# Performance work log

Measured on AMD Instinct MI355X. Metric: run time of the kernel, lower is better.

The kernel has to match this reference:

```python
import jax, jax.numpy as jnp
import numpy as np

GROUP_SIZE = 128

def dequantize(imatrix, scales, zeros, group_size, out_dtype):
    # repeat group-wise scales/zeros along axis 0 to full weight shape
    rs = jnp.repeat(scales, group_size, axis=0)
    rz = jnp.repeat(zeros, group_size, axis=0)
    return ((imatrix.astype(rs.dtype) - rz.astype(rs.dtype)) * rs).astype(out_dtype)

def setup_inputs() -> dict:
    key = jax.random.key(0)
    ks = jax.random.split(key, 10)
    H, I, G = 4096, 14336, GROUP_SIZE
    B, S = 4, 2048
    x = jax.random.normal(ks[0], (B, S, H), dtype=jnp.float32)
    gate_w = jax.random.randint(ks[1], (H, I), 0, 16, dtype=jnp.int32)
    gate_z = jax.random.randint(ks[2], (H // G, I), 0, 16, dtype=jnp.int32)
    gate_s = jax.random.uniform(ks[3], (H // G, I), dtype=jnp.float32) * 0.01
    up_w = jax.random.randint(ks[4], (H, I), 0, 16, dtype=jnp.int32)
    up_z = jax.random.randint(ks[5], (H // G, I), 0, 16, dtype=jnp.int32)
    up_s = jax.random.uniform(ks[6], (H // G, I), dtype=jnp.float32) * 0.01
    down_w = jax.random.randint(ks[7], (I, H), 0, 16, dtype=jnp.int32)
    down_z = jax.random.randint(ks[8], (I // G, H), 0, 16, dtype=jnp.int32)
    down_s = jax.random.uniform(ks[9], (I // G, H), dtype=jnp.float32) * 0.01
    return {"x": x, "gate_w": gate_w, "gate_z": gate_z, "gate_s": gate_s,
            "up_w": up_w, "up_z": up_z, "up_s": up_s,
            "down_w": down_w, "down_z": down_z, "down_s": down_s}

def reference(x, gate_w, gate_z, gate_s, up_w, up_z, up_s, down_w, down_z, down_s):
    dt = x.dtype
    gate_proj = dequantize(gate_w, gate_s, gate_z, GROUP_SIZE, dt)  # [H, I]
    up_proj = dequantize(up_w, up_s, up_z, GROUP_SIZE, dt)          # [H, I]
    down_proj = dequantize(down_w, down_s, down_z, GROUP_SIZE, dt)  # [I, H]
    gate = jax.nn.silu(jnp.dot(x, gate_proj))  # [B, S, I]
    up = jnp.dot(x, up_proj)                   # [B, S, I]
    return jnp.dot(gate * up, down_proj)       # [B, S, H]
```

## Files before the change

### kernel.cpp

```cpp
#include <hip/hip_runtime.h>
#include <cstdint>
#include <cstddef>

typedef unsigned short u16;
typedef unsigned int u32;
typedef float f32x4 __attribute__((ext_vector_type(4)));
typedef __bf16 bf16x8 __attribute__((ext_vector_type(8)));

__device__ inline u16 f32_to_bf16(float f) {
  u32 u = __float_as_uint(f);
  u = (u + 0x7FFFu + ((u >> 16) & 1u)) >> 16;
  return (u16)u;
}

#define GLD16(src, dst)                                                        \
  __builtin_amdgcn_global_load_lds(                                            \
      (const __attribute__((address_space(1))) u32*)(src),                     \
      (__attribute__((address_space(3))) u32*)(dst), 16, 0, 0)

#define SBAR() __builtin_amdgcn_s_barrier()
#define SETPRIO(x) __builtin_amdgcn_s_setprio(x)
#define WAIT_LGKM0()                                                           \
  do {                                                                         \
    asm volatile("s_waitcnt lgkmcnt(0)" ::: "memory");                         \
    __builtin_amdgcn_sched_barrier(0);                                         \
  } while (0)
#define WAITV(N) asm volatile("s_waitcnt vmcnt(" #N ")" ::: "memory")
#define MFMA16(a, b, c) __builtin_amdgcn_mfma_f32_16x16x32_bf16(a, b, c, 0, 0, 0)

__device__ inline void stage_op(const char* src, void* ldsBase, int rowBase,
                                int wave) {
  GLD16(src, (char*)ldsBase + rowBase * 128 + wave * 1024);
}

__device__ inline bf16x8 fragK(const u16* tile, int row, int ks, int p) {
  const int byte = row * 128 + (((ks << 6) + (p << 4)) ^ ((row & 7) << 4));
  return *(const bf16x8*)((const char*)tile + byte);
}

__global__ void k_convert_x(const float* __restrict__ x, u16* __restrict__ o) {
  const long i = (long)blockIdx.x * 256 + threadIdx.x;
  const float4 a = ((const float4*)x)[i * 2];
  const float4 b = ((const float4*)x)[i * 2 + 1];
  uint4 r;
  r.x = (u32)f32_to_bf16(a.x) | ((u32)f32_to_bf16(a.y) << 16);
  r.y = (u32)f32_to_bf16(a.z) | ((u32)f32_to_bf16(a.w) << 16);
  r.z = (u32)f32_to_bf16(b.x) | ((u32)f32_to_bf16(b.y) << 16);
  r.w = (u32)f32_to_bf16(b.z) | ((u32)f32_to_bf16(b.w) << 16);
  ((uint4*)o)[i] = r;
}

__global__ __launch_bounds__(256) void k_dequant(const int* __restrict__ W,
                                                 const int* __restrict__ Z,
                                                 const float* __restrict__ S,
                                                 u16* __restrict__ out, int K,
                                                 int N) {
  __shared__ u16 ldsT[256 * 66];
  const int k0 = blockIdx.x * 64, n0 = blockIdx.y * 256;
  const int t = threadIdx.x;
  const int n4 = t & 63;
  const int kr = t >> 6;
  const int g = k0 >> 7;
  const int nb = n0 + n4 * 4;
  const int4 z4 = *(const int4*)(Z + (size_t)g * N + nb);
  const float4 s4 = *(const float4*)(S + (size_t)g * N + nb);
#pragma unroll
  for (int pass = 0; pass < 16; ++pass) {
    const int kl = kr + pass * 4;
    const int4 w4 = *(const int4*)(W + (size_t)(k0 + kl) * N + nb);
    ldsT[(n4 * 4 + 0) * 66 + kl] = f32_to_bf16((float)(w4.x - z4.x) * s4.x);
    ldsT[(n4 * 4 + 1) * 66 + kl] = f32_to_bf16((float)(w4.y - z4.y) * s4.y);
    ldsT[(n4 * 4 + 2) * 66 + kl] = f32_to_bf16((float)(w4.z - z4.z) * s4.z);
    ldsT[(n4 * 4 + 3) * 66 + kl] = f32_to_bf16((float)(w4.w - z4.w) * s4.w);
  }
  __syncthreads();
#pragma unroll
  for (int pass = 0; pass < 8; ++pass) {
    const int nl = pass * 32 + (t >> 3);
    const int kc = (t & 7) * 8;
    const u16* p = &ldsT[nl * 66 + kc];
    const u32 w0 = *(const u32*)(p + 0);
    const u32 w1 = *(const u32*)(p + 2);
    const u32 w2 = *(const u32*)(p + 4);
    const u32 w3 = *(const u32*)(p + 6);
    *(uint4*)(out + (size_t)(n0 + nl) * K + k0 + kc) =
        make_uint4(w0, w1, w2, w3);
  }
}

__global__ __launch_bounds__(512, 2) void k_gemm_gu(
    const u16* __restrict__ X, const u16* __restrict__ WG,
    const u16* __restrict__ WU, u16* __restrict__ Hout) {
  __shared__ __align__(16) u16 lA[2][16384];
  __shared__ __align__(16) u16 lG[2][8192];
  __shared__ __align__(16) u16 lU[2][8192];
  const int NKT = 64;
  const int m0 = blockIdx.x * 256, n0 = blockIdx.y * 128;
  const int tid = threadIdx.x, lane = tid & 63, wave = tid >> 6;
  const int p = lane >> 4, r16 = lane & 15;
  const int wr = wave >> 2, wc = wave & 3;

  const int srow = tid >> 3;
  const int skb = (((tid ^ (tid >> 3)) & 7) << 4);
  const char* baA = (const char*)X + (long)(m0 + srow) * 8192 + skb;
  const char* baG = (const char*)WG + (long)(n0 + srow) * 8192 + skb;
  const char* baU = (const char*)WU + (long)(n0 + srow) * 8192 + skb;

#define ISS_A(kt2, rb) \
  stage_op(baA + (long)(rb) * 8192 + (long)(kt2) * 128, lA[(kt2) & 1], rb, wave)
#define ISS_G(kt2, rb) \
  stage_op(baG + (long)(rb) * 8192 + (long)(kt2) * 128, lG[(kt2) & 1], rb, wave)
#define ISS_U(kt2, rb) \
  stage_op(baU + (long)(rb) * 8192 + (long)(kt2) * 128, lU[(kt2) & 1], rb, wave)

  f32x4 aG[8][2], aU[8][2];
  const f32x4 zero = {0.f, 0.f, 0.f, 0.f};
#pragma unroll
  for (int i = 0; i < 8; ++i)
#pragma unroll
    for (int j = 0; j < 2; ++j) {
      aG[i][j] = zero;
      aU[i][j] = zero;
    }

  ISS_A(0, 0); ISS_A(0, 128);
  ISS_G(0, 0); ISS_G(0, 64);
  ISS_U(0, 0); ISS_U(0, 64);
  ISS_A(1, 0); ISS_A(1, 128);
  ISS_A(0, 64); ISS_A(0, 192);
  WAITV(4);
  SBAR();

  for (int kt = 0; kt < NKT; ++kt) {
    const int b = kt & 1;
    const u16* hA = lA[b];
    const u16* hG = lG[b];
    const u16* hU = lU[b];
    bf16x8 af[2][4], gf[2][2], uf[2][2], ah[2][4];
#pragma unroll
    for (int ks = 0; ks < 2; ++ks) {
#pragma unroll
      for (int ii = 0; ii < 4; ++ii)
        af[ks][ii] = fragK(hA, wr * 128 + ii * 16 + r16, ks, p);
#pragma unroll
      for (int j = 0; j < 2; ++j)
        gf[ks][j] = fragK(hG, wc * 32 + j * 16 + r16, ks, p);
    }
    if (kt < NKT - 1) { ISS_G(kt + 1, 0); ISS_G(kt + 1, 64); }
    SETPRIO(1);
#pragma unroll
    for (int ks = 0; ks < 2; ++ks)
#pragma unroll
      for (int ii = 0; ii < 4; ++ii)
#pragma unroll
        for (int j = 0; j < 2; ++j)
          aG[ii][j] = MFMA16(af[ks][ii], gf[ks][j], aG[ii][j]);
    SETPRIO(0);
#pragma unroll
    for (int ks = 0; ks < 2; ++ks)
#pragma unroll
      for (int j = 0; j < 2; ++j)
        uf[ks][j] = fragK(hU, wc * 32 + j * 16 + r16, ks, p);
    if (kt < NKT - 1) { ISS_U(kt + 1, 0); ISS_U(kt + 1, 64); }
    SETPRIO(1);
#pragma unroll
    for (int ks = 0; ks < 2; ++ks)
#pragma unroll
      for (int ii = 0; ii < 4; ++ii)
#pragma unroll
        for (int j = 0; j < 2; ++j)
          aU[ii][j] = MFMA16(af[ks][ii], uf[ks][j], aU[ii][j]);
    SETPRIO(0);
    WAIT_LGKM0();
    if (kt < NKT - 1) WAITV(4); else WAITV(0);
    SBAR();
    if (kt < NKT - 2) { ISS_A(kt + 2, 0); ISS_A(kt + 2, 128); }
#pragma unroll
    for (int ks = 0; ks < 2; ++ks)
#pragma unroll
      for (int ii = 0; ii < 4; ++ii)
        ah[ks][ii] = fragK(hA, wr * 128 + 64 + ii * 16 + r16, ks, p);
    if (kt < NKT - 1) { ISS_A(kt + 1, 64); ISS_A(kt + 1, 192); }
    SETPRIO(1);
#pragma unroll
    for (int ks = 0; ks < 2; ++ks)
#pragma unroll
      for (int ii = 0; ii < 4; ++ii)
#pragma unroll
        for (int j = 0; j < 2; ++j)
          aG[4 + ii][j] = MFMA16(ah[ks][ii], gf[ks][j], aG[4 + ii][j]);
#pragma unroll
    for (int ks = 0; ks < 2; ++ks)
#pragma unroll
      for (int ii = 0; ii < 4; ++ii)
#pragma unroll
        for (int j = 0; j < 2; ++j)
          aU[4 + ii][j] = MFMA16(ah[ks][ii], uf[ks][j], aU[4 + ii][j]);
    SETPRIO(0);
    if (kt < NKT - 2) WAITV(4);
    else if (kt == NKT - 2) WAITV(2);
    SBAR();
  }
#undef ISS_A
#undef ISS_G
#undef ISS_U

#pragma unroll
  for (int i = 0; i < 8; ++i) {
    const int row = m0 + wr * 128 + i * 16 + p * 4;
#pragma unroll
    for (int j = 0; j < 2; ++j) {
      const int col = n0 + wc * 32 + j * 16 + r16;
      u16* dst = Hout + (size_t)row * 14336 + col;
#pragma unroll
      for (int r = 0; r < 4; ++r) {
        const float gv = aG[i][j][r], uv = aU[i][j][r];
        const float sv = gv / (1.f + __expf(-gv)) * uv;
        dst[(size_t)r * 14336] = f32_to_bf16(sv);
      }
    }
  }
}

__global__ __launch_bounds__(512, 2) void k_gemm_down(
    const u16* __restrict__ Hin, const u16* __restrict__ WD,
    float* __restrict__ Out) {
  __shared__ __align__(16) u16 lA[2][16384];
  __shared__ __align__(16) u16 lB[2][16384];
  const int NKT = 224;
  const int m0 = blockIdx.x * 256, n0 = blockIdx.y * 256;
  const int tid = threadIdx.x, lane = tid & 63, wave = tid >> 6;
  const int p = lane >> 4, r16 = lane & 15;
  const int wr = wave >> 2, wc = wave & 3;

  const int srow = tid >> 3;
  const int skb = (((tid ^ (tid >> 3)) & 7) << 4);
  const char* baA = (const char*)Hin + (long)(m0 + srow) * 28672 + skb;
  const char* baB = (const char*)WD + (long)(n0 + srow) * 28672 + skb;

#define ISS_A(kt2, rb) \
  stage_op(baA + (long)(rb) * 28672 + (long)(kt2) * 128, lA[(kt2) & 1], rb, wave)
#define ISS_B(kt2, rb) \
  stage_op(baB + (long)(rb) * 28672 + (long)(kt2) * 128, lB[(kt2) & 1], rb, wave)

  f32x4 acc[8][4];
  const f32x4 zero = {0.f, 0.f, 0.f, 0.f};
#pragma unroll
  for (int i = 0; i < 8; ++i)
#pragma unroll
    for (int j = 0; j < 4; ++j) acc[i][j] = zero;

  ISS_A(0, 0); ISS_A(0, 128);
  ISS_B(0, 0); ISS_B(0, 64); ISS_B(0, 128); ISS_B(0, 192);
  ISS_A(1, 0); ISS_A(1, 128);
  ISS_A(0, 64); ISS_A(0, 192);
  WAITV(4);
  SBAR();

  for (int kt = 0; kt < NKT; ++kt) {
    const int b = kt & 1;
    const u16* hA = lA[b];
    const u16* hB = lB[b];
    bf16x8 af[2][4], bfr[2][4], ah[2][4];
#pragma unroll
    for (int ks = 0; ks < 2; ++ks) {
#pragma unroll
      for (int ii = 0; ii < 4; ++ii)
        af[ks][ii] = fragK(hA, wr * 128 + ii * 16 + r16, ks, p);
#pragma unroll
      for (int j = 0; j < 4; ++j)
        bfr[ks][j] = fragK(hB, wc * 64 + j * 16 + r16, ks, p);
    }
    if (kt < NKT - 1) {
      ISS_B(kt + 1, 0); ISS_B(kt + 1, 64);
      ISS_B(kt + 1, 128); ISS_B(kt + 1, 192);
    }
    SETPRIO(1);
#pragma unroll
    for (int ks = 0; ks < 2; ++ks)
#pragma unroll
      for (int ii = 0; ii < 4; ++ii)
#pragma unroll
        for (int j = 0; j < 4; ++j)
          acc[ii][j] = MFMA16(af[ks][ii], bfr[ks][j], acc[ii][j]);
    SETPRIO(0);
    WAIT_LGKM0();
    if (kt < NKT - 1) WAITV(4); else WAITV(0);
    SBAR();
    if (kt < NKT - 2) { ISS_A(kt + 2, 0); ISS_A(kt + 2, 128); }
#pragma unroll
    for (int ks = 0; ks < 2; ++ks)
#pragma unroll
      for (int ii = 0; ii < 4; ++ii)
        ah[ks][ii] = fragK(hA, wr * 128 + 64 + ii * 16 + r16, ks, p);
    if (kt < NKT - 1) { ISS_A(kt + 1, 64); ISS_A(kt + 1, 192); }
    SETPRIO(1);
#pragma unroll
    for (int ks = 0; ks < 2; ++ks)
#pragma unroll
      for (int ii = 0; ii < 4; ++ii)
#pragma unroll
        for (int j = 0; j < 4; ++j)
          acc[4 + ii][j] = MFMA16(ah[ks][ii], bfr[ks][j], acc[4 + ii][j]);
    SETPRIO(0);
    if (kt < NKT - 2) WAITV(4);
    else if (kt == NKT - 2) WAITV(2);
    SBAR();
  }
#undef ISS_A
#undef ISS_B

#pragma unroll
  for (int i = 0; i < 8; ++i) {
    const int row = m0 + wr * 128 + i * 16 + p * 4;
#pragma unroll
    for (int j = 0; j < 4; ++j) {
      const int col = n0 + wc * 64 + j * 16 + r16;
      float* dst = Out + (size_t)row * 4096 + col;
#pragma unroll
      for (int r = 0; r < 4; ++r) dst[(size_t)r * 4096] = acc[i][j][r];
    }
  }
}

__global__ void k_fill(float* o, long n, float v) {
  const long i = (long)blockIdx.x * 256 + threadIdx.x;
  if (i < n) o[i] = v;
}

extern "C" void kernel_launch(void* const* d_in, const int* in_sizes, int n_in,
                              void* d_out, int out_size, void* d_ws,
                              size_t ws_size, hipStream_t stream) {
  const float* x = (const float*)d_in[0];
  const int* gw = (const int*)d_in[1];
  const int* gz = (const int*)d_in[2];
  const float* gs = (const float*)d_in[3];
  const int* uw = (const int*)d_in[4];
  const int* uz = (const int*)d_in[5];
  const float* us = (const float*)d_in[6];
  const int* dw = (const int*)d_in[7];
  const int* dz = (const int*)d_in[8];
  const float* dsc = (const float*)d_in[9];
  float* out = (float*)d_out;

  const size_t NX = 33554432UL, NW = 58720256UL;
  const size_t need = 2UL * (NX + 3UL * NW + 117440512UL);
  if (ws_size < need) {
    k_fill<<<(out_size + 255) / 256, 256, 0, stream>>>(out, out_size, 1.0e6f);
    return;
  }
  u16* wsx = (u16*)d_ws;
  u16* wgq = wsx + NX;
  u16* wuq = wgq + NW;
  u16* wdq = wuq + NW;
  u16* wh = wdq + NW;

  k_convert_x<<<16384, 256, 0, stream>>>(x, wsx);
  dim3 dq1(64, 56);
  k_dequant<<<dq1, 256, 0, stream>>>(gw, gz, gs, wgq, 4096, 14336);
  k_dequant<<<dq1, 256, 0, stream>>>(uw, uz, us, wuq, 4096, 14336);
  dim3 dq2(224, 16);
  k_dequant<<<dq2, 256, 0, stream>>>(dw, dz, dsc, wdq, 14336, 4096);
  dim3 g1(32, 112);
  k_gemm_gu<<<g1, 512, 0, stream>>>(wsx, wgq, wuq, wh);
  dim3 g2(32, 16);
  k_gemm_down<<<g2, 512, 0, stream>>>(wh, wdq, out);
}
```

Measured before the change: 2.777 ms.

## Unfuse gate/up GEMM into generic 256x256 GEMM with finer-grained LDS pipeline

Replaces the fused gate+up GEMM with two launches of a templated 256x256 GEMM. Each launch writes bf16 gate or up activations, and a separate elementwise kernel then applies SiLU and the multiply. The main loop is re-split into four quarter-MFMA phases with extra barriers so B and A fragment loads interleave with the MFMAs, and the dequantised weight buffer is reused across projections. This trades the fused epilogue and shared X tile loads for larger tiles and a more balanced schedule, at the cost of extra global traffic for the gate/up intermediates and more barriers.

Result: slower. 2.868 ms (+3.3%).

```diff
diff --git a/kernel.cpp b/kernel.cpp
--- a/kernel.cpp
+++ b/kernel.cpp
@@ -11,6 +11,10 @@
   u32 u = __float_as_uint(f);
   u = (u + 0x7FFFu + ((u >> 16) & 1u)) >> 16;
   return (u16)u;
+}
+__device__ inline float bf16_to_f32(u16 h) {
+  u32 u = (u32)h << 16;
+  return __uint_as_float(u);
 }
 
 #define GLD16(src, dst)                                                        \
@@ -88,146 +92,14 @@
   }
 }
 
-__global__ __launch_bounds__(512, 2) void k_gemm_gu(
-    const u16* __restrict__ X, const u16* __restrict__ WG,
-    const u16* __restrict__ WU, u16* __restrict__ Hout) {
-  __shared__ __align__(16) u16 lA[2][16384];
-  __shared__ __align__(16) u16 lG[2][8192];
-  __shared__ __align__(16) u16 lU[2][8192];
-  const int NKT = 64;
-  const int m0 = blockIdx.x * 256, n0 = blockIdx.y * 128;
-  const int tid = threadIdx.x, lane = tid & 63, wave = tid >> 6;
-  const int p = lane >> 4, r16 = lane & 15;
-  const int wr = wave >> 2, wc = wave & 3;
-
-  const int srow = tid >> 3;
-  const int skb = (((tid ^ (tid >> 3)) & 7) << 4);
-  const char* baA = (const char*)X + (long)(m0 + srow) * 8192 + skb;
-  const char* baG = (const char*)WG + (long)(n0 + srow) * 8192 + skb;
-  const char* baU = (const char*)WU + (long)(n0 + srow) * 8192 + skb;
-
-#define ISS_A(kt2, rb) \
-  stage_op(baA + (long)(rb) * 8192 + (long)(kt2) * 128, lA[(kt2) & 1], rb, wave)
-#define ISS_G(kt2, rb) \
-  stage_op(baG + (long)(rb) * 8192 + (long)(kt2) * 128, lG[(kt2) & 1], rb, wave)
-#define ISS_U(kt2, rb) \
-  stage_op(baU + (long)(rb) * 8192 + (long)(kt2) * 128, lU[(kt2) & 1], rb, wave)
-
-  f32x4 aG[8][2], aU[8][2];
-  const f32x4 zero = {0.f, 0.f, 0.f, 0.f};
-#pragma unroll
-  for (int i = 0; i < 8; ++i)
-#pragma unroll
-    for (int j = 0; j < 2; ++j) {
-      aG[i][j] = zero;
-      aU[i][j] = zero;
-    }
-
-  ISS_A(0, 0); ISS_A(0, 128);
-  ISS_G(0, 0); ISS_G(0, 64);
-  ISS_U(0, 0); ISS_U(0, 64);
-  ISS_A(1, 0); ISS_A(1, 128);
-  ISS_A(0, 64); ISS_A(0, 192);
-  WAITV(4);
-  SBAR();
-
-  for (int kt = 0; kt < NKT; ++kt) {
-    const int b = kt & 1;
-    const u16* hA = lA[b];
-    const u16* hG = lG[b];
-    const u16* hU = lU[b];
-    bf16x8 af[2][4], gf[2][2], uf[2][2], ah[2][4];
-#pragma unroll
-    for (int ks = 0; ks < 2; ++ks) {
-#pragma unroll
-      for (int ii = 0; ii < 4; ++ii)
-        af[ks][ii] = fragK(hA, wr * 128 + ii * 16 + r16, ks, p);
-#pragma unroll
-      for (int j = 0; j < 2; ++j)
-        gf[ks][j] = fragK(hG, wc * 32 + j * 16 + r16, ks, p);
-    }
-    if (kt < NKT - 1) { ISS_G(kt + 1, 0); ISS_G(kt + 1, 64); }
-    SETPRIO(1);
-#pragma unroll
-    for (int ks = 0; ks < 2; ++ks)
-#pragma unroll
-      for (int ii = 0; ii < 4; ++ii)
-#pragma unroll
-        for (int j = 0; j < 2; ++j)
-          aG[ii][j] = MFMA16(af[ks][ii], gf[ks][j], aG[ii][j]);
-    SETPRIO(0);
-#pragma unroll
-    for (int ks = 0; ks < 2; ++ks)
-#pragma unroll
-      for (int j = 0; j < 2; ++j)
-        uf[ks][j] = fragK(hU, wc * 32 + j * 16 + r16, ks, p);
-    if (kt < NKT - 1) { ISS_U(kt + 1, 0); ISS_U(kt + 1, 64); }
-    SETPRIO(1);
-#pragma unroll
-    for (int ks = 0; ks < 2; ++ks)
-#pragma unroll
-      for (int ii = 0; ii < 4; ++ii)
-#pragma unroll
-        for (int j = 0; j < 2; ++j)
-          aU[ii][j] = MFMA16(af[ks][ii], uf[ks][j], aU[ii][j]);
-    SETPRIO(0);
-    WAIT_LGKM0();
-    if (kt < NKT - 1) WAITV(4); else WAITV(0);
-    SBAR();
-    if (kt < NKT - 2) { ISS_A(kt + 2, 0); ISS_A(kt + 2, 128); }
-#pragma unroll
-    for (int ks = 0; ks < 2; ++ks)
-#pragma unroll
-      for (int ii = 0; ii < 4; ++ii)
-        ah[ks][ii] = fragK(hA, wr * 128 + 64 + ii * 16 + r16, ks, p);
-    if (kt < NKT - 1) { ISS_A(kt + 1, 64); ISS_A(kt + 1, 192); }
-    SETPRIO(1);
-#pragma unroll
-    for (int ks = 0; ks < 2; ++ks)
-#pragma unroll
-      for (int ii = 0; ii < 4; ++ii)
-#pragma unroll
-        for (int j = 0; j < 2; ++j)
-          aG[4 + ii][j] = MFMA16(ah[ks][ii], gf[ks][j], aG[4 + ii][j]);
-#pragma unroll
-    for (int ks = 0; ks < 2; ++ks)
-#pragma unroll
-      for (int ii = 0; ii < 4; ++ii)
-#pragma unroll
-        for (int j = 0; j < 2; ++j)
-          aU[4 + ii][j] = MFMA16(ah[ks][ii], uf[ks][j], aU[4 + ii][j]);
-    SETPRIO(0);
-    if (kt < NKT - 2) WAITV(4);
-    else if (kt == NKT - 2) WAITV(2);
-    SBAR();
-  }
-#undef ISS_A
-#undef ISS_G
-#undef ISS_U
-
-#pragma unroll
-  for (int i = 0; i < 8; ++i) {
-    const int row = m0 + wr * 128 + i * 16 + p * 4;
-#pragma unroll
-    for (int j = 0; j < 2; ++j) {
-      const int col = n0 + wc * 32 + j * 16 + r16;
-      u16* dst = Hout + (size_t)row * 14336 + col;
-#pragma unroll
-      for (int r = 0; r < 4; ++r) {
-        const float gv = aG[i][j][r], uv = aU[i][j][r];
-        const float sv = gv / (1.f + __expf(-gv)) * uv;
-        dst[(size_t)r * 14336] = f32_to_bf16(sv);
-      }
-    }
-  }
-}
-
-__global__ __launch_bounds__(512, 2) void k_gemm_down(
-    const u16* __restrict__ Hin, const u16* __restrict__ WD,
-    float* __restrict__ Out) {
+template <int NKT, bool OUT_BF16>
+__global__ __launch_bounds__(512, 2) void k_gemm(const u16* __restrict__ A,
+                                                 const u16* __restrict__ B,
+                                                 void* __restrict__ OutP,
+                                                 int ldOut) {
   __shared__ __align__(16) u16 lA[2][16384];
   __shared__ __align__(16) u16 lB[2][16384];
-  const int NKT = 224;
+  const long STRB = (long)NKT * 128;
   const int m0 = blockIdx.x * 256, n0 = blockIdx.y * 256;
   const int tid = threadIdx.x, lane = tid & 63, wave = tid >> 6;
   const int p = lane >> 4, r16 = lane & 15;
@@ -235,13 +107,13 @@
 
   const int srow = tid >> 3;
   const int skb = (((tid ^ (tid >> 3)) & 7) << 4);
-  const char* baA = (const char*)Hin + (long)(m0 + srow) * 28672 + skb;
-  const char* baB = (const char*)WD + (long)(n0 + srow) * 28672 + skb;
+  const char* baA = (const char*)A + (long)(m0 + srow) * STRB + skb;
+  const char* baB = (const char*)B + (long)(n0 + srow) * STRB + skb;
 
 #define ISS_A(kt2, rb) \
-  stage_op(baA + (long)(rb) * 28672 + (long)(kt2) * 128, lA[(kt2) & 1], rb, wave)
+  stage_op(baA + (long)(rb)*STRB + (long)(kt2) * 128, lA[(kt2) & 1], rb, wave)
 #define ISS_B(kt2, rb) \
-  stage_op(baB + (long)(rb) * 28672 + (long)(kt2) * 128, lB[(kt2) & 1], rb, wave)
+  stage_op(baB + (long)(rb)*STRB + (long)(kt2) * 128, lB[(kt2) & 1], rb, wave)
 
   f32x4 acc[8][4];
   const f32x4 zero = {0.f, 0.f, 0.f, 0.f};
@@ -250,10 +122,9 @@
 #pragma unroll
     for (int j = 0; j < 4; ++j) acc[i][j] = zero;
 
-  ISS_A(0, 0); ISS_A(0, 128);
-  ISS_B(0, 0); ISS_B(0, 64); ISS_B(0, 128); ISS_B(0, 192);
+  ISS_A(0, 0); ISS_A(0, 128); ISS_B(0, 0); ISS_B(0, 64);
+  ISS_B(0, 128); ISS_B(0, 192); ISS_A(0, 64); ISS_A(0, 192);
   ISS_A(1, 0); ISS_A(1, 128);
-  ISS_A(0, 64); ISS_A(0, 192);
   WAITV(4);
   SBAR();
 
@@ -261,47 +132,76 @@
     const int b = kt & 1;
     const u16* hA = lA[b];
     const u16* hB = lB[b];
-    bf16x8 af[2][4], bfr[2][4], ah[2][4];
+    bf16x8 af[2][4], bfr[2][4];
 #pragma unroll
     for (int ks = 0; ks < 2; ++ks) {
 #pragma unroll
       for (int ii = 0; ii < 4; ++ii)
         af[ks][ii] = fragK(hA, wr * 128 + ii * 16 + r16, ks, p);
 #pragma unroll
-      for (int j = 0; j < 4; ++j)
+      for (int j = 0; j < 2; ++j)
         bfr[ks][j] = fragK(hB, wc * 64 + j * 16 + r16, ks, p);
     }
-    if (kt < NKT - 1) {
-      ISS_B(kt + 1, 0); ISS_B(kt + 1, 64);
-      ISS_B(kt + 1, 128); ISS_B(kt + 1, 192);
-    }
-    SETPRIO(1);
-#pragma unroll
-    for (int ks = 0; ks < 2; ++ks)
-#pragma unroll
-      for (int ii = 0; ii < 4; ++ii)
-#pragma unroll
-        for (int j = 0; j < 4; ++j)
+    if (kt < NKT - 1) { ISS_B(kt + 1, 0); ISS_B(kt + 1, 64); }
+    SBAR();
+    WAIT_LGKM0();
+    SETPRIO(1);
+#pragma unroll
+    for (int ks = 0; ks < 2; ++ks)
+#pragma unroll
+      for (int ii = 0; ii < 4; ++ii)
+#pragma unroll
+        for (int j = 0; j < 2; ++j)
           acc[ii][j] = MFMA16(af[ks][ii], bfr[ks][j], acc[ii][j]);
     SETPRIO(0);
+    SBAR();
+#pragma unroll
+    for (int ks = 0; ks < 2; ++ks)
+#pragma unroll
+      for (int j = 2; j < 4; ++j)
+        bfr[ks][j] = fragK(hB, wc * 64 + j * 16 + r16, ks, p);
+    if (kt < NKT - 1) { ISS_B(kt + 1, 128); ISS_B(kt + 1, 192); }
+    SBAR();
     WAIT_LGKM0();
-    if (kt < NKT - 1) WAITV(4); else WAITV(0);
+    SETPRIO(1);
+#pragma unroll
+    for (int ks = 0; ks < 2; ++ks)
+#pragma unroll
+      for (int ii = 0; ii < 4; ++ii)
+#pragma unroll
+        for (int j = 2; j < 4; ++j)
+          acc[ii][j] = MFMA16(af[ks][ii], bfr[ks][j], acc[ii][j]);
+    SETPRIO(0);
+    if (kt < NKT - 1) WAITV(6); else WAITV(0);
+    SBAR();
+#pragma unroll
+    for (int ks = 0; ks < 2; ++ks)
+#pragma unroll
+      for (int ii = 0; ii < 4; ++ii)
+        af[ks][ii] = fragK(hA, wr * 128 + 64 + ii * 16 + r16, ks, p);
+    if (kt < NKT - 1) { ISS_A(kt + 1, 64); ISS_A(kt + 1, 192); }
+    SBAR();
+    WAIT_LGKM0();
+    SETPRIO(1);
+#pragma unroll
+    for (int ks = 0; ks < 2; ++ks)
+#pragma unroll
+      for (int ii = 0; ii < 4; ++ii)
+#pragma unroll
+        for (int j = 0; j < 2; ++j)
+          acc[4 + ii][j] = MFMA16(af[ks][ii], bfr[ks][j], acc[4 + ii][j]);
+    SETPRIO(0);
     SBAR();
     if (kt < NKT - 2) { ISS_A(kt + 2, 0); ISS_A(kt + 2, 128); }
-#pragma unroll
-    for (int ks = 0; ks < 2; ++ks)
-#pragma unroll
-      for (int ii = 0; ii < 4; ++ii)
-        ah[ks][ii] = fragK(hA, wr * 128 + 64 + ii * 16 + r16, ks, p);
-    if (kt < NKT - 1) { ISS_A(kt + 1, 64); ISS_A(kt + 1, 192); }
-    SETPRIO(1);
-#pragma unroll
-    for (int ks = 0; ks < 2; ++ks)
-#pragma unroll
-      for (int ii = 0; ii < 4; ++ii)
-#pragma unroll
-        for (int j = 0; j < 4; ++j)
-          acc[4 + ii][j] = MFMA16(ah[ks][ii], bfr[ks][j], acc[4 + ii][j]);
+    SBAR();
+    SETPRIO(1);
+#pragma unroll
+    for (int ks = 0; ks < 2; ++ks)
+#pragma unroll
+      for (int ii = 0; ii < 4; ++ii)
+#pragma unroll
+        for (int j = 2; j < 4; ++j)
+          acc[4 + ii][j] = MFMA16(af[ks][ii], bfr[ks][j], acc[4 + ii][j]);
     SETPRIO(0);
     if (kt < NKT - 2) WAITV(4);
     else if (kt == NKT - 2) WAITV(2);
@@ -316,11 +216,38 @@
 #pragma unroll
     for (int j = 0; j < 4; ++j) {
       const int col = n0 + wc * 64 + j * 16 + r16;
-      float* dst = Out + (size_t)row * 4096 + col;
-#pragma unroll
-      for (int r = 0; r < 4; ++r) dst[(size_t)r * 4096] = acc[i][j][r];
+      if constexpr (OUT_BF16) {
+        u16* dst = (u16*)OutP + (size_t)row * ldOut + col;
+#pragma unroll
+        for (int r = 0; r < 4; ++r)
+          dst[(size_t)r * ldOut] = f32_to_bf16(acc[i][j][r]);
+      } else {
+        float* dst = (float*)OutP + (size_t)row * ldOut + col;
+#pragma unroll
+        for (int r = 0; r < 4; ++r) dst[(size_t)r * ldOut] = acc[i][j][r];
+      }
     }
   }
+}
+
+__global__ __launch_bounds__(256) void k_silu_mul(u16* __restrict__ g,
+                                                  const u16* __restrict__ u) {
+  const long i = (long)blockIdx.x * 256 + threadIdx.x;
+  uint4 gv = ((const uint4*)g)[i];
+  const uint4 uv = ((const uint4*)u)[i];
+  u32* gw = (u32*)&gv;
+  const u32* uw = (const u32*)&uv;
+#pragma unroll
+  for (int q = 0; q < 4; ++q) {
+    const float g0 = bf16_to_f32((u16)(gw[q] & 0xFFFF));
+    const float g1 = bf16_to_f32((u16)(gw[q] >> 16));
+    const float u0 = bf16_to_f32((u16)(uw[q] & 0xFFFF));
+    const float u1 = bf16_to_f32((u16)(uw[q] >> 16));
+    const float h0 = g0 / (1.f + __expf(-g0)) * u0;
+    const float h1 = g1 / (1.f + __expf(-g1)) * u1;
+    gw[q] = (u32)f32_to_bf16(h0) | ((u32)f32_to_bf16(h1) << 16);
+  }
+  ((uint4*)g)[i] = gv;
 }
 
 __global__ void k_fill(float* o, long n, float v) {
@@ -343,26 +270,29 @@
   const float* dsc = (const float*)d_in[9];
   float* out = (float*)d_out;
 
-  const size_t NX = 33554432UL, NW = 58720256UL;
-  const size_t need = 2UL * (NX + 3UL * NW + 117440512UL);
+  const size_t NX = 33554432UL, NW = 58720256UL, NH = 117440512UL;
+  const size_t need = 2UL * (NX + NW + 2UL * NH);
   if (ws_size < need) {
     k_fill<<<(out_size + 255) / 256, 256, 0, stream>>>(out, out_size, 1.0e6f);
     return;
   }
   u16* wsx = (u16*)d_ws;
-  u16* wgq = wsx + NX;
-  u16* wuq = wgq + NW;
-  u16* wdq = wuq + NW;
-  u16* wh = wdq + NW;
+  u16* wW = wsx + NX;
+  u16* wg = wW + NW;
+  u16* wu = wg + NH;
 
   k_convert_x<<<16384, 256, 0, stream>>>(x, wsx);
+
   dim3 dq1(64, 56);
-  k_dequant<<<dq1, 256, 0, stream>>>(gw, gz, gs, wgq, 4096, 14336);
-  k_dequant<<<dq1, 256, 0, stream>>>(uw, uz, us, wuq, 4096, 14336);
   dim3 dq2(224, 16);
-  k_dequant<<<dq2, 256, 0, stream>>>(dw, dz, dsc, wdq, 14336, 4096);
-  dim3 g1(32, 112);
-  k_gemm_gu<<<g1, 512, 0, stream>>>(wsx, wgq, wuq, wh);
-  dim3 g2(32, 16);
-  k_gemm_down<<<g2, 512, 0, stream>>>(wh, wdq, out);
-}
+  dim3 gUp(32, 56);
+  dim3 gDn(32, 16);
+
+  k_dequant<<<dq1, 256, 0, stream>>>(gw, gz, gs, wW, 4096, 14336);
+  k_gemm<64, true><<<gUp, 512, 0, stream>>>(wsx, wW, wg, 14336);
+  k_dequant<<<dq1, 256, 0, stream>>>(uw, uz, us, wW, 4096, 14336);
+  k_gemm<64, true><<<gUp, 512, 0, stream>>>(wsx, wW, wu, 14336);
+  k_silu_mul<<<57344, 256, 0, stream>>>(wg, wu);
+  k_dequant<<<dq2, 256, 0, stream>>>(dw, dz, dsc, wW, 14336, 4096);
+  k_gemm<224, false><<<gDn, 512, 0, stream>>>(wg, wW, out, 4096);
+}
```
